# Optimization experiments

Measured on AMD Instinct MI355X. Metric: run time of the kernel, lower is better.

The kernel has to match this reference:

```python
import jax, jax.numpy as jnp
import numpy as np

H = 4096          # hidden_size
NH = 32           # num_attention_heads
NKV = 2           # multi_query_group_num (kv heads)
HD = 128          # kv_channels / head_dim
RD = 64           # rotary_dim = head_dim * rotary_percent(0.5)
T = 2048          # total tokens (single prefill sequence)
EPS = 1e-5        # layernorm_epsilon
ROPE_BASE = 10000.0


def setup_inputs() -> dict:
    key = jax.random.key(0)
    k0, k1, k2, k3 = jax.random.split(key, 4)
    qkv_out = (NH + 2 * NKV) * HD  # 4608
    return {
        "positions": jnp.arange(T, dtype=jnp.int32),
        "hidden_states": jax.random.normal(k0, (T, H), jnp.float32),
        "w_qkv": jax.random.normal(k1, (qkv_out, H), jnp.float32) * 0.02,
        "b_qkv": jax.random.normal(k2, (qkv_out,), jnp.float32) * 0.02,
        "w_dense": jax.random.normal(k3, (H, NH * HD), jnp.float32) * 0.02,
        "q_ln_w": jnp.ones((HD,), jnp.float32),
        "k_ln_w": jnp.ones((HD,), jnp.float32),
    }


def _rmsnorm(x, w):
    # per-head RMSNorm over head_dim
    return x * jax.lax.rsqrt(jnp.mean(x * x, axis=-1, keepdims=True) + EPS) * w


def _rope(x, positions):
    # partial rotary (first RD dims), interleaved GPT-J style (is_neox_style=False)
    inv_freq = 1.0 / (ROPE_BASE ** (jnp.arange(0, RD, 2, dtype=jnp.float32) / RD))
    ang = positions.astype(jnp.float32)[:, None] * inv_freq      # [T, RD//2]
    cos = jnp.cos(ang)[:, None, :]                               # [T, 1, RD//2]
    sin = jnp.sin(ang)[:, None, :]
    x_rot, x_pass = x[..., :RD], x[..., RD:]
    x1 = x_rot[..., 0::2]
    x2 = x_rot[..., 1::2]
    r1 = x1 * cos - x2 * sin
    r2 = x2 * cos + x1 * sin
    x_rot = jnp.stack([r1, r2], axis=-1).reshape(x.shape[:-1] + (RD,))
    return jnp.concatenate([x_rot, x_pass], axis=-1)


def reference(positions, hidden_states, w_qkv, b_qkv, w_dense, q_ln_w, k_ln_w):
    qkv = hidden_states @ w_qkv.T + b_qkv                        # [T, 4608]
    q_size, kv_size = NH * HD, NKV * HD
    q = qkv[:, :q_size].reshape(T, NH, HD)
    k = qkv[:, q_size:q_size + kv_size].reshape(T, NKV, HD)
    v = qkv[:, q_size + kv_size:].reshape(T, NKV, HD)
    # optional qk layernorm (RMSNorm since config.rmsnorm)
    q = _rmsnorm(q, q_ln_w)
    k = _rmsnorm(k, k_ln_w)
    # rotary embedding
    q = _rope(q, positions)
    k = _rope(k, positions)
    # GQA: expand kv heads to query heads
    group = NH // NKV
    k_exp = jnp.repeat(k, group, axis=1)                         # [T, NH, HD]
    v_exp = jnp.repeat(v, group, axis=1)
    scale = HD ** -0.5
    scores = jnp.einsum("thd,shd->hts", q, k_exp) * scale        # [NH, T, T]
    causal = jnp.tril(jnp.ones((T, T), dtype=bool))
    scores = jnp.where(causal[None, :, :], scores, jnp.finfo(scores.dtype).min)
    attn = jax.nn.softmax(scores, axis=-1)
    out = jnp.einsum("hts,shd->thd", attn, v_exp).reshape(T, NH * HD)
    return out @ w_dense.T                                       # [T, H]
```

## Files before the change

kernel.cpp:

```cpp
#include <hip/hip_runtime.h>
#include <cstdint>
#include <cstddef>

typedef short short4v __attribute__((ext_vector_type(4)));
typedef short short8v __attribute__((ext_vector_type(8)));
typedef float f32x4   __attribute__((ext_vector_type(4)));

#define T_LEN  2048
#define HDIM   4096
#define NHEADS 32
#define HEADD  128
#define QKVN   4608

static __device__ __forceinline__ short f2bf(float f) {
  __bf16 h = (__bf16)f;
  return __builtin_bit_cast(short, h);
}
static __device__ __forceinline__ float bf2f(short u) {
  return __builtin_bit_cast(float, ((unsigned int)(unsigned short)u) << 16);
}

static __device__ __forceinline__ void gload_lds16(const void* g, void* l) {
  __builtin_amdgcn_global_load_lds((const __attribute__((address_space(1))) void*)g,
                                   (__attribute__((address_space(3))) void*)l,
                                   16, 0, 0);
}

__global__ void cast_pair(const float* __restrict__ a, short* __restrict__ oa, int na4,
                          const float* __restrict__ b, short* __restrict__ ob, int nb4) {
  int idx = blockIdx.x * blockDim.x + threadIdx.x;
  int stride = gridDim.x * blockDim.x;
  const int ntot = na4 + nb4;
  for (int i = idx; i < ntot; i += stride) {
    const float4* src = (i < na4) ? ((const float4*)a + i) : ((const float4*)b + (i - na4));
    short4v* dst      = (i < na4) ? ((short4v*)oa + i)     : ((short4v*)ob + (i - na4));
    float4 v = *src;
    short4v o;
    o[0] = f2bf(v.x); o[1] = f2bf(v.y); o[2] = f2bf(v.z); o[3] = f2bf(v.w);
    *dst = o;
  }
}

__global__ void cast_f32_to_bf16(const float* __restrict__ in, short* __restrict__ out, int n4) {
  int idx = blockIdx.x * blockDim.x + threadIdx.x;
  int stride = gridDim.x * blockDim.x;
  const float4* in4 = (const float4*)in;
  short4v* out4 = (short4v*)out;
  for (int i = idx; i < n4; i += stride) {
    float4 v = in4[i];
    short4v o;
    o[0] = f2bf(v.x); o[1] = f2bf(v.y); o[2] = f2bf(v.z); o[3] = f2bf(v.w);
    out4[i] = o;
  }
}

template <int OUT_BF16>
__global__ __launch_bounds__(256, 2) void gemm_bt(
    const short* __restrict__ A,
    const short* __restrict__ B,
    const float* __restrict__ bias,
    void* __restrict__ Cout,
    int M, int N, int K)
{
  __shared__ short sA[128 * 64];
  __shared__ short sB[128 * 64];
  const int tid  = threadIdx.x;
  const int lane = tid & 63;
  const int wv   = tid >> 6;
  const int wr   = wv >> 1;
  const int wc   = wv & 1;

  const int nwg  = gridDim.x * gridDim.y;
  int wgid = blockIdx.y * gridDim.x + blockIdx.x;
  wgid = (wgid & 7) * (nwg >> 3) + (wgid >> 3);
  const int bn0 = (wgid / gridDim.y) * 128;
  const int bm0 = (wgid % gridDim.y) * 128;

  const int fr  = lane & 15;
  const int fkb = (lane >> 4) << 4;
  const int swz = (fr & 7) << 4;

  const int c_row  = tid >> 3;
  const int c_colb = (tid & 7) << 4;
  const int c_scol = (c_colb ^ ((c_row & 7) << 4)) >> 1;

  auto STAGE = [&](int kt) {
#pragma unroll
    for (int i = 0; i < 4; i++) {
      const int row = i * 32 + c_row;
      gload_lds16(A + (size_t)(bm0 + row) * K + kt + c_scol,
                  (char*)sA + (size_t)(i * 256 + wv * 64) * 16);
      gload_lds16(B + (size_t)(bn0 + row) * K + kt + c_scol,
                  (char*)sB + (size_t)(i * 256 + wv * 64) * 16);
    }
  };

  f32x4 zero = {0.f, 0.f, 0.f, 0.f};
  f32x4 acc[4][4];
#pragma unroll
  for (int m = 0; m < 4; m++)
#pragma unroll
    for (int n = 0; n < 4; n++) acc[m][n] = zero;

  for (int kt = 0; kt < K; kt += 64) {
    STAGE(kt);
    __syncthreads();
    const char* aB = (const char*)sA;
    const char* bB = (const char*)sB;
#pragma unroll
    for (int ks = 0; ks < 2; ks++) {
      short8v af[4], bfr[4];
#pragma unroll
      for (int m = 0; m < 4; m++) {
        const int row = wr * 64 + m * 16 + fr;
        af[m] = *(const short8v*)(aB + row * 128 + ((ks * 64 + fkb) ^ swz));
      }
#pragma unroll
      for (int n = 0; n < 4; n++) {
        const int row = wc * 64 + n * 16 + fr;
        bfr[n] = *(const short8v*)(bB + row * 128 + ((ks * 64 + fkb) ^ swz));
      }
#pragma unroll
      for (int m = 0; m < 4; m++)
#pragma unroll
        for (int n = 0; n < 4; n++)
          acc[m][n] = __builtin_amdgcn_mfma_f32_16x16x32_bf16(af[m], bfr[n], acc[m][n], 0, 0, 0);
    }
    __syncthreads();
  }

  const int rg = (lane >> 4) * 4;
#pragma unroll
  for (int m = 0; m < 4; m++) {
#pragma unroll
    for (int n = 0; n < 4; n++) {
      const int gcol = bn0 + wc * 64 + n * 16 + fr;
      const float bv = bias ? bias[gcol] : 0.0f;
#pragma unroll
      for (int j = 0; j < 4; j++) {
        const int grow = bm0 + wr * 64 + m * 16 + rg + j;
        const float v = acc[m][n][j] + bv;
        if (OUT_BF16)
          ((short*)Cout)[(size_t)grow * N + gcol] = f2bf(v);
        else
          ((float*)Cout)[(size_t)grow * N + gcol] = v;
      }
    }
  }
}

__global__ __launch_bounds__(256) void qkv_post_kernel(
    const short* __restrict__ qkvb,
    const int*   __restrict__ positions,
    const float* __restrict__ q_ln,
    const float* __restrict__ k_ln,
    short* __restrict__ Qb,
    short* __restrict__ Kb,
    short* __restrict__ Vt)
{
  const int t = blockIdx.x;
  const int h = blockIdx.y * 4 + (threadIdx.x >> 6);
  const int lane = threadIdx.x & 63;
  const unsigned int pk =
      ((const unsigned int*)(qkvb + (size_t)t * QKVN + h * HEADD))[lane];
  float x = bf2f((short)(pk & 0xffffu));
  float y = bf2f((short)(pk >> 16));

  if (h >= 34) {
    const int hv = h - 34;
    short* dst = Vt + ((size_t)hv * HEADD + 2 * lane) * T_LEN + t;
    dst[0]     = f2bf(x);
    dst[T_LEN] = f2bf(y);
    return;
  }

  float ss = x * x + y * y;
#pragma unroll
  for (int d = 32; d > 0; d >>= 1) ss += __shfl_xor(ss, d);
  const float r = rsqrtf(ss * (1.0f / 128.0f) + 1e-5f);
  const float* lnw = (h < 32) ? q_ln : k_ln;
  x = x * r * lnw[2 * lane];
  y = y * r * lnw[2 * lane + 1];

  if (lane < 32) {
    const float pos = (float)positions[t];
    const float ang = pos * powf(10000.0f, -(float)lane * (1.0f / 32.0f));
    const float c = cosf(ang), s = sinf(ang);
    const float r1 = x * c - y * s;
    const float r2 = y * c + x * s;
    x = r1; y = r2;
  }

  short* dst = (h < 32) ? (Qb + ((size_t)h * T_LEN + t) * HEADD + 2 * lane)
                        : (Kb + ((size_t)(h - 32) * T_LEN + t) * HEADD + 2 * lane);
  dst[0] = f2bf(x);
  dst[1] = f2bf(y);
}

__global__ __launch_bounds__(256, 2) void attn_kernel(
    const short* __restrict__ Qb,
    const short* __restrict__ Kb,
    const short* __restrict__ Vt,
    short* __restrict__ attn_out)
{
  __shared__ short Ks[2][64 * 128];
  __shared__ short Vs[2][128 * 64];
  __shared__ short pbuf[4][32 * 64];
  const int blk  = gridDim.x - 1 - blockIdx.x;
  const int h    = blockIdx.y;
  const int hkv  = h >> 4;
  const int tid  = threadIdx.x;
  const int lane = tid & 63;
  const int wv   = tid >> 6;
  const int B0   = blk * 128;
  const int qrow0 = B0 + wv * 32;
  const int fr = lane & 15;
  const int fk = (lane >> 4) * 8;
  const int fkb = (lane >> 4) << 4;
  const int rg = (lane >> 4) * 4;
  const int swz = (fr & 7) << 4;

  const short* Kh = Kb + (size_t)hkv * T_LEN * HEADD;
  const short* Vh = Vt + (size_t)hkv * HEADD * T_LEN;

  short8v qf[2][4];
#pragma unroll
  for (int g = 0; g < 2; g++) {
    const short* Qrow = Qb + ((size_t)h * T_LEN + qrow0 + g * 16 + fr) * HEADD + fk;
#pragma unroll
    for (int d0 = 0; d0 < 4; d0++) qf[g][d0] = *(const short8v*)(Qrow + d0 * 32);
  }

  float mrow[2][4], lrow[2][4];
#pragma unroll
  for (int g = 0; g < 2; g++)
#pragma unroll
    for (int j = 0; j < 4; j++) { mrow[g][j] = -1e30f; lrow[g][j] = 0.f; }
  f32x4 zero = {0.f, 0.f, 0.f, 0.f};
  f32x4 o[2][8];
#pragma unroll
  for (int g = 0; g < 2; g++)
#pragma unroll
    for (int d = 0; d < 8; d++) o[g][d] = zero;

  char* pb = (char*)&pbuf[wv][0];
  const float scale = 0.08838834764831845f;
  const int nt = 2 * blk + 2;

  auto STAGE = [&](int b, int t) {
    const int s0 = t * 64;
#pragma unroll
    for (int i = 0; i < 4; i++) {
      const int c    = i * 256 + tid;
      const int row  = c >> 4;
      const int colb = (c & 15) << 4;
      const int scol = (colb ^ ((row & 7) << 4)) >> 1;
      gload_lds16(Kh + (size_t)(s0 + row) * HEADD + scol,
                  (char*)&Ks[b][0] + (size_t)(i * 256 + wv * 64) * 16);
    }
#pragma unroll
    for (int i = 0; i < 4; i++) {
      const int c    = i * 256 + tid;
      const int row  = c >> 3;
      const int colb = (c & 7) << 4;
      const int scol = (colb ^ ((row & 7) << 4)) >> 1;
      gload_lds16(Vh + (size_t)row * T_LEN + s0 + scol,
                  (char*)&Vs[b][0] + (size_t)(i * 256 + wv * 64) * 16);
    }
  };

  int cur = 0;
  STAGE(0, 0);
  __syncthreads();

  for (int t = 0; t < nt; ++t) {
    if (t + 1 < nt) STAGE(cur ^ 1, t + 1);
    const int s0 = t * 64;
    const char* KsB = (const char*)&Ks[cur][0];
    const char* VsB = (const char*)&Vs[cur][0];

    float scv[2][4][4];
#pragma unroll
    for (int sub = 0; sub < 4; sub++) {
      const char* Kbase = KsB + (sub * 16 + fr) * 256;
      f32x4 a0 = zero, a1 = zero;
#pragma unroll
      for (int d0 = 0; d0 < 4; d0++) {
        short8v kf = *(const short8v*)(Kbase + ((d0 * 64 + fkb) ^ swz));
        a0 = __builtin_amdgcn_mfma_f32_16x16x32_bf16(qf[0][d0], kf, a0, 0, 0, 0);
        a1 = __builtin_amdgcn_mfma_f32_16x16x32_bf16(qf[1][d0], kf, a1, 0, 0, 0);
      }
#pragma unroll
      for (int j = 0; j < 4; j++) {
        scv[0][sub][j] = a0[j] * scale;
        scv[1][sub][j] = a1[j] * scale;
      }
    }
    if (t >= nt - 2) {
#pragma unroll
      for (int g = 0; g < 2; g++)
#pragma unroll
        for (int sub = 0; sub < 4; sub++) {
          const int colp = s0 + sub * 16 + fr;
#pragma unroll
          for (int j = 0; j < 4; j++)
            if (colp > qrow0 + g * 16 + rg + j) scv[g][sub][j] = -1e30f;
        }
    }
    float pmax[2][4];
#pragma unroll
    for (int g = 0; g < 2; g++)
#pragma unroll
      for (int j = 0; j < 4; j++)
        pmax[g][j] = fmaxf(fmaxf(scv[g][0][j], scv[g][1][j]),
                           fmaxf(scv[g][2][j], scv[g][3][j]));
    float growth = -1e30f;
#pragma unroll
    for (int g = 0; g < 2; g++)
#pragma unroll
      for (int j = 0; j < 4; j++) growth = fmaxf(growth, pmax[g][j] - mrow[g][j]);
    if (!__all(growth <= 8.0f)) {
#pragma unroll
      for (int g = 0; g < 2; g++)
#pragma unroll
        for (int j = 0; j < 4; j++) {
          float mx = pmax[g][j];
#pragma unroll
          for (int d = 1; d < 16; d <<= 1) mx = fmaxf(mx, __shfl_xor(mx, d));
          const float mn = fmaxf(mrow[g][j], mx);
          const float c  = __expf(mrow[g][j] - mn);
          mrow[g][j] = mn;
          lrow[g][j] *= c;
#pragma unroll
          for (int df = 0; df < 8; df++) o[g][df][j] *= c;
        }
    }
#pragma unroll
    for (int g = 0; g < 2; g++)
#pragma unroll
      for (int j = 0; j < 4; j++) {
        const int prow = g * 16 + rg + j;
        char* prb = pb + prow * 128;
        const int rswz = ((rg + j) & 7) << 4;
        float ps = 0.f;
#pragma unroll
        for (int sub = 0; sub < 4; sub++) {
          const float p = __expf(scv[g][sub][j] - mrow[g][j]);
          ps += p;
          *(short*)(prb + ((((sub * 16 + fr) << 1)) ^ rswz)) = f2bf(p);
        }
        lrow[g][j] += ps;
      }
    asm volatile("" ::: "memory");
    short8v pf[2][2];
#pragma unroll
    for (int g = 0; g < 2; g++)
#pragma unroll
      for (int ks = 0; ks < 2; ks++)
        pf[g][ks] = *(const short8v*)(pb + (g * 16 + fr) * 128 + ((ks * 64 + fkb) ^ swz));
#pragma unroll
    for (int df = 0; df < 8; df++) {
      const char* Vbase = VsB + (df * 16 + fr) * 128;
      short8v vf0 = *(const short8v*)(Vbase + ((0 + fkb) ^ swz));
      short8v vf1 = *(const short8v*)(Vbase + ((64 + fkb) ^ swz));
      o[0][df] = __builtin_amdgcn_mfma_f32_16x16x32_bf16(pf[0][0], vf0, o[0][df], 0, 0, 0);
      o[0][df] = __builtin_amdgcn_mfma_f32_16x16x32_bf16(pf[0][1], vf1, o[0][df], 0, 0, 0);
      o[1][df] = __builtin_amdgcn_mfma_f32_16x16x32_bf16(pf[1][0], vf0, o[1][df], 0, 0, 0);
      o[1][df] = __builtin_amdgcn_mfma_f32_16x16x32_bf16(pf[1][1], vf1, o[1][df], 0, 0, 0);
    }
    __syncthreads();
    cur ^= 1;
  }

#pragma unroll
  for (int g = 0; g < 2; g++)
#pragma unroll
    for (int j = 0; j < 4; j++) {
#pragma unroll
      for (int d = 1; d < 16; d <<= 1) lrow[g][j] += __shfl_xor(lrow[g][j], d);
    }
#pragma unroll
  for (int g = 0; g < 2; g++)
#pragma unroll
    for (int df = 0; df < 8; df++)
#pragma unroll
      for (int j = 0; j < 4; j++) {
        const float v = o[g][df][j] / lrow[g][j];
        attn_out[(size_t)(qrow0 + g * 16 + rg + j) * HDIM + h * HEADD + df * 16 + fr] = f2bf(v);
      }
}

extern "C" void kernel_launch(void* const* d_in, const int* in_sizes, int n_in,
                              void* d_out, int out_size, void* d_ws, size_t ws_size,
                              hipStream_t stream) {
  (void)out_size; (void)ws_size;
  int ip = 0, ih = 1, iwq = 2, ib = 3, iwd = 4, il0 = 5, il1 = 6;
  if (n_in == 7) {
    int p = -1, hh = -1, wq = -1, b = -1, wd = -1, l0 = -1, l1 = -1, ok = 1;
    for (int i = 0; i < 7; i++) {
      switch (in_sizes[i]) {
        case 2048:     p  = i; break;
        case 8388608:  hh = i; break;
        case 18874368: wq = i; break;
        case 4608:     b  = i; break;
        case 16777216: wd = i; break;
        case 128:      if (l0 < 0) l0 = i; else l1 = i; break;
        default:       ok = 0; break;
      }
    }
    if (ok && p >= 0 && hh >= 0 && wq >= 0 && b >= 0 && wd >= 0 && l0 >= 0 && l1 >= 0) {
      ip = p; ih = hh; iwq = wq; ib = b; iwd = wd; il0 = l0; il1 = l1;
    }
  }

  const int*   positions = (const int*)d_in[ip];
  const float* hidden    = (const float*)d_in[ih];
  const float* w_qkv     = (const float*)d_in[iwq];
  const float* b_qkv     = (const float*)d_in[ib];
  const float* w_dense   = (const float*)d_in[iwd];
  const float* q_ln      = (const float*)d_in[il0];
  const float* k_ln      = (const float*)d_in[il1];

  char* ws = (char*)d_ws;
  short* Ahs   = (short*)(ws + 0);
  short* Qb    = (short*)(ws + 0);
  short* Wqkv  = (short*)(ws + (size_t)16777216);
  short* Kb    = (short*)(ws + (size_t)16777216);
  short* Vt    = (short*)(ws + (size_t)17825792);
  short* Wd    = (short*)(ws + (size_t)18874368);
  short* qkvb  = (short*)(ws + (size_t)54525952);
  short* attnb = (short*)(ws + (size_t)54525952);

  cast_pair<<<dim3(3072), dim3(256), 0, stream>>>(
      hidden, Ahs, (T_LEN * HDIM) / 4, w_qkv, Wqkv, (QKVN * HDIM) / 4);
  gemm_bt<1><<<dim3(QKVN / 128, T_LEN / 128), dim3(256), 0, stream>>>(
      Ahs, Wqkv, b_qkv, (void*)qkvb, T_LEN, QKVN, HDIM);
  qkv_post_kernel<<<dim3(T_LEN, 9), dim3(256), 0, stream>>>(
      qkvb, positions, q_ln, k_ln, Qb, Kb, Vt);
  cast_f32_to_bf16<<<dim3(2048), dim3(256), 0, stream>>>(w_dense, Wd, (HDIM * HDIM) / 4);
  attn_kernel<<<dim3(16, NHEADS), dim3(256), 0, stream>>>(Qb, Kb, Vt, attnb);
  gemm_bt<0><<<dim3(HDIM / 128, T_LEN / 128), dim3(256), 0, stream>>>(
      attnb, Wd, nullptr, d_out, T_LEN, HDIM, HDIM);
}
```

Baseline: 316.2 us.

## Pair early and late query tiles per block to balance causal attention work

Each attention block now handles two 64-row query chunks, one from the start and one from the end of the sequence (x and 31-x), so every block processes roughly the same number of causal KV tiles. This removes the load imbalance where late blocks did far more work than early ones. The early chunk's MFMAs and softmax run only while the KV tile index is within its causal range, which adds branches inside the inner loop. The launch grid must change to 16 blocks per head for this mapping to be correct.

```diff
diff --git a/kernel.cpp b/kernel.cpp
--- a/kernel.cpp
+++ b/kernel.cpp
@@ -206,14 +206,15 @@
   __shared__ short Ks[2][64 * 128];
   __shared__ short Vs[2][128 * 64];
   __shared__ short pbuf[4][32 * 64];
-  const int blk  = gridDim.x - 1 - blockIdx.x;
+  const int x    = blockIdx.x;
   const int h    = blockIdx.y;
   const int hkv  = h >> 4;
   const int tid  = threadIdx.x;
   const int lane = tid & 63;
   const int wv   = tid >> 6;
-  const int B0   = blk * 128;
-  const int qrow0 = B0 + wv * 32;
+  const int qA   = x * 64 + wv * 16;
+  const int qB   = (31 - x) * 64 + wv * 16;
+  const int nt   = 32 - x;
   const int fr = lane & 15;
   const int fk = (lane >> 4) * 8;
   const int fkb = (lane >> 4) << 4;
@@ -223,12 +224,15 @@
   const short* Kh = Kb + (size_t)hkv * T_LEN * HEADD;
   const short* Vh = Vt + (size_t)hkv * HEADD * T_LEN;
 
-  short8v qf[2][4];
-#pragma unroll
-  for (int g = 0; g < 2; g++) {
-    const short* Qrow = Qb + ((size_t)h * T_LEN + qrow0 + g * 16 + fr) * HEADD + fk;
-#pragma unroll
-    for (int d0 = 0; d0 < 4; d0++) qf[g][d0] = *(const short8v*)(Qrow + d0 * 32);
+  short8v qf0[4], qf1[4];
+  {
+    const short* QrowA = Qb + ((size_t)h * T_LEN + qA + fr) * HEADD + fk;
+    const short* QrowB = Qb + ((size_t)h * T_LEN + qB + fr) * HEADD + fk;
+#pragma unroll
+    for (int d0 = 0; d0 < 4; d0++) {
+      qf0[d0] = *(const short8v*)(QrowA + d0 * 32);
+      qf1[d0] = *(const short8v*)(QrowB + d0 * 32);
+    }
   }
 
   float mrow[2][4], lrow[2][4];
@@ -245,7 +249,6 @@
 
   char* pb = (char*)&pbuf[wv][0];
   const float scale = 0.08838834764831845f;
-  const int nt = 2 * blk + 2;
 
   auto STAGE = [&](int b, int t) {
     const int s0 = t * 64;
@@ -276,10 +279,11 @@
   for (int t = 0; t < nt; ++t) {
     if (t + 1 < nt) STAGE(cur ^ 1, t + 1);
     const int s0 = t * 64;
+    const bool dual = (t <= x);
     const char* KsB = (const char*)&Ks[cur][0];
     const char* VsB = (const char*)&Vs[cur][0];
 
-    float scv[2][4][4];
+    float scv0[4][4], scv1[4][4];
 #pragma unroll
     for (int sub = 0; sub < 4; sub++) {
       const char* Kbase = KsB + (sub * 16 + fr) * 256;
@@ -287,86 +291,121 @@
 #pragma unroll
       for (int d0 = 0; d0 < 4; d0++) {
         short8v kf = *(const short8v*)(Kbase + ((d0 * 64 + fkb) ^ swz));
-        a0 = __builtin_amdgcn_mfma_f32_16x16x32_bf16(qf[0][d0], kf, a0, 0, 0, 0);
-        a1 = __builtin_amdgcn_mfma_f32_16x16x32_bf16(qf[1][d0], kf, a1, 0, 0, 0);
+        a1 = __builtin_amdgcn_mfma_f32_16x16x32_bf16(qf1[d0], kf, a1, 0, 0, 0);
+        if (dual) a0 = __builtin_amdgcn_mfma_f32_16x16x32_bf16(qf0[d0], kf, a0, 0, 0, 0);
       }
 #pragma unroll
       for (int j = 0; j < 4; j++) {
-        scv[0][sub][j] = a0[j] * scale;
-        scv[1][sub][j] = a1[j] * scale;
-      }
-    }
-    if (t >= nt - 2) {
-#pragma unroll
-      for (int g = 0; g < 2; g++)
+        scv1[sub][j] = a1[j] * scale;
+        scv0[sub][j] = a0[j] * scale;
+      }
+    }
+    if (t == x) {
+#pragma unroll
+      for (int sub = 0; sub < 4; sub++) {
+        const int colp = s0 + sub * 16 + fr;
+#pragma unroll
+        for (int j = 0; j < 4; j++)
+          if (colp > qA + rg + j) scv0[sub][j] = -1e30f;
+      }
+    }
+    if (t == nt - 1) {
+#pragma unroll
+      for (int sub = 0; sub < 4; sub++) {
+        const int colp = s0 + sub * 16 + fr;
+#pragma unroll
+        for (int j = 0; j < 4; j++)
+          if (colp > qB + rg + j) scv1[sub][j] = -1e30f;
+      }
+    }
+    float pmax1[4], pmax0[4];
+#pragma unroll
+    for (int j = 0; j < 4; j++)
+      pmax1[j] = fmaxf(fmaxf(scv1[0][j], scv1[1][j]), fmaxf(scv1[2][j], scv1[3][j]));
+    float growth = -1e30f;
+#pragma unroll
+    for (int j = 0; j < 4; j++) growth = fmaxf(growth, pmax1[j] - mrow[1][j]);
+    if (dual) {
+#pragma unroll
+      for (int j = 0; j < 4; j++) {
+        pmax0[j] = fmaxf(fmaxf(scv0[0][j], scv0[1][j]), fmaxf(scv0[2][j], scv0[3][j]));
+        growth = fmaxf(growth, pmax0[j] - mrow[0][j]);
+      }
+    }
+    if (!__all(growth <= 8.0f)) {
+#pragma unroll
+      for (int j = 0; j < 4; j++) {
+        float mx = pmax1[j];
+#pragma unroll
+        for (int d = 1; d < 16; d <<= 1) mx = fmaxf(mx, __shfl_xor(mx, d));
+        const float mn = fmaxf(mrow[1][j], mx);
+        const float c  = __expf(mrow[1][j] - mn);
+        mrow[1][j] = mn;
+        lrow[1][j] *= c;
+#pragma unroll
+        for (int df = 0; df < 8; df++) o[1][df][j] *= c;
+      }
+      if (dual) {
+#pragma unroll
+        for (int j = 0; j < 4; j++) {
+          float mx = pmax0[j];
+#pragma unroll
+          for (int d = 1; d < 16; d <<= 1) mx = fmaxf(mx, __shfl_xor(mx, d));
+          const float mn = fmaxf(mrow[0][j], mx);
+          const float c  = __expf(mrow[0][j] - mn);
+          mrow[0][j] = mn;
+          lrow[0][j] *= c;
+#pragma unroll
+          for (int df = 0; df < 8; df++) o[0][df][j] *= c;
+        }
+      }
+    }
+#pragma unroll
+    for (int j = 0; j < 4; j++) {
+      const int rswz = ((rg + j) & 7) << 4;
+      char* prb1 = pb + (16 + rg + j) * 128;
+      float ps1 = 0.f;
+#pragma unroll
+      for (int sub = 0; sub < 4; sub++) {
+        const float p = __expf(scv1[sub][j] - mrow[1][j]);
+        ps1 += p;
+        *(short*)(prb1 + ((((sub * 16 + fr) << 1)) ^ rswz)) = f2bf(p);
+      }
+      lrow[1][j] += ps1;
+    }
+    if (dual) {
+#pragma unroll
+      for (int j = 0; j < 4; j++) {
+        const int rswz = ((rg + j) & 7) << 4;
+        char* prb0 = pb + (rg + j) * 128;
+        float ps0 = 0.f;
 #pragma unroll
         for (int sub = 0; sub < 4; sub++) {
-          const int colp = s0 + sub * 16 + fr;
-#pragma unroll
-          for (int j = 0; j < 4; j++)
-            if (colp > qrow0 + g * 16 + rg + j) scv[g][sub][j] = -1e30f;
+          const float p = __expf(scv0[sub][j] - mrow[0][j]);
+          ps0 += p;
+          *(short*)(prb0 + ((((sub * 16 + fr) << 1)) ^ rswz)) = f2bf(p);
         }
-    }
-    float pmax[2][4];
-#pragma unroll
-    for (int g = 0; g < 2; g++)
-#pragma unroll
-      for (int j = 0; j < 4; j++)
-        pmax[g][j] = fmaxf(fmaxf(scv[g][0][j], scv[g][1][j]),
-                           fmaxf(scv[g][2][j], scv[g][3][j]));
-    float growth = -1e30f;
-#pragma unroll
-    for (int g = 0; g < 2; g++)
-#pragma unroll
-      for (int j = 0; j < 4; j++) growth = fmaxf(growth, pmax[g][j] - mrow[g][j]);
-    if (!__all(growth <= 8.0f)) {
-#pragma unroll
-      for (int g = 0; g < 2; g++)
-#pragma unroll
-        for (int j = 0; j < 4; j++) {
-          float mx = pmax[g][j];
-#pragma unroll
-          for (int d = 1; d < 16; d <<= 1) mx = fmaxf(mx, __shfl_xor(mx, d));
-          const float mn = fmaxf(mrow[g][j], mx);
-          const float c  = __expf(mrow[g][j] - mn);
-          mrow[g][j] = mn;
-          lrow[g][j] *= c;
-#pragma unroll
-          for (int df = 0; df < 8; df++) o[g][df][j] *= c;
-        }
-    }
-#pragma unroll
-    for (int g = 0; g < 2; g++)
-#pragma unroll
-      for (int j = 0; j < 4; j++) {
-        const int prow = g * 16 + rg + j;
-        char* prb = pb + prow * 128;
-        const int rswz = ((rg + j) & 7) << 4;
-        float ps = 0.f;
-#pragma unroll
-        for (int sub = 0; sub < 4; sub++) {
-          const float p = __expf(scv[g][sub][j] - mrow[g][j]);
-          ps += p;
-          *(short*)(prb + ((((sub * 16 + fr) << 1)) ^ rswz)) = f2bf(p);
-        }
-        lrow[g][j] += ps;
-      }
+        lrow[0][j] += ps0;
+      }
+    }
     asm volatile("" ::: "memory");
-    short8v pf[2][2];
-#pragma unroll
-    for (int g = 0; g < 2; g++)
-#pragma unroll
-      for (int ks = 0; ks < 2; ks++)
-        pf[g][ks] = *(const short8v*)(pb + (g * 16 + fr) * 128 + ((ks * 64 + fkb) ^ swz));
+    short8v pf1[2], pf0[2];
+#pragma unroll
+    for (int ks = 0; ks < 2; ks++) {
+      pf1[ks] = *(const short8v*)(pb + (16 + fr) * 128 + ((ks * 64 + fkb) ^ swz));
+      pf0[ks] = *(const short8v*)(pb + fr * 128 + ((ks * 64 + fkb) ^ swz));
+    }
 #pragma unroll
     for (int df = 0; df < 8; df++) {
       const char* Vbase = VsB + (df * 16 + fr) * 128;
       short8v vf0 = *(const short8v*)(Vbase + ((0 + fkb) ^ swz));
       short8v vf1 = *(const short8v*)(Vbase + ((64 + fkb) ^ swz));
-      o[0][df] = __builtin_amdgcn_mfma_f32_16x16x32_bf16(pf[0][0], vf0, o[0][df], 0, 0, 0);
-      o[0][df] = __builtin_amdgcn_mfma_f32_16x16x32_bf16(pf[0][1], vf1, o[0][df], 0, 0, 0);
-      o[1][df] = __builtin_amdgcn_mfma_f32_16x16x32_bf16(pf[1][0], vf0, o[1][df], 0, 0, 0);
-      o[1][df] = __builtin_amdgcn_mfma_f32_16x16x32_bf16(pf[1][1], vf1, o[1][df], 0, 0, 0);
+      o[1][df] = __builtin_amdgcn_mfma_f32_16x16x32_bf16(pf1[0], vf0, o[1][df], 0, 0, 0);
+      o[1][df] = __builtin_amdgcn_mfma_f32_16x16x32_bf16(pf1[1], vf1, o[1][df], 0, 0, 0);
+      if (dual) {
+        o[0][df] = __builtin_amdgcn_mfma_f32_16x16x32_bf16(pf0[0], vf0, o[0][df], 0, 0, 0);
+        o[0][df] = __builtin_amdgcn_mfma_f32_16x16x32_bf16(pf0[1], vf1, o[0][df], 0, 0, 0);
+      }
     }
     __syncthreads();
     cur ^= 1;
@@ -380,14 +419,14 @@
       for (int d = 1; d < 16; d <<= 1) lrow[g][j] += __shfl_xor(lrow[g][j], d);
     }
 #pragma unroll
-  for (int g = 0; g < 2; g++)
-#pragma unroll
-    for (int df = 0; df < 8; df++)
-#pragma unroll
-      for (int j = 0; j < 4; j++) {
-        const float v = o[g][df][j] / lrow[g][j];
-        attn_out[(size_t)(qrow0 + g * 16 + rg + j) * HDIM + h * HEADD + df * 16 + fr] = f2bf(v);
-      }
+  for (int df = 0; df < 8; df++)
+#pragma unroll
+    for (int j = 0; j < 4; j++) {
+      const float v0 = o[0][df][j] / lrow[0][j];
+      attn_out[(size_t)(qA + rg + j) * HDIM + h * HEADD + df * 16 + fr] = f2bf(v0);
+      const float v1 = o[1][df][j] / lrow[1][j];
+      attn_out[(size_t)(qB + rg + j) * HDIM + h * HEADD + df * 16 + fr] = f2bf(v1);
+    }
 }
 
 extern "C" void kernel_launch(void* const* d_in, const int* in_sizes, int n_in,
```

New measurement: 308.0 us. -2.6%, faster.
